# Optimization experiments

Measured on AMD Instinct MI355X. Metric: run time of the kernel, lower is better.

The kernel has to match this reference:

```python
import jax, jax.numpy as jnp
import numpy as np

NQ = 6          # num_qubits
BS = 3          # basis_size (Pauli x,y,z)
HID = 32        # LSTM hidden size
SNAPS = 16      # max_num_snapshots
BATCH = 1024
DIM = 2 ** NQ   # 64


def _pauli():
    sx = np.array([[0., 1.], [1., 0.]], dtype=np.complex64)
    sy = np.array([[0., -1j], [1j, 0.]], dtype=np.complex64)
    sz = np.array([[1., 0.], [0., -1.]], dtype=np.complex64)
    return np.stack([sx, sy, sz], axis=0)


def setup_inputs():
    key = jax.random.key(0)
    ks = jax.random.split(key, 12)
    snapshot = jax.random.uniform(ks[0], (BATCH, NQ), jnp.float32, -1.0, 1.0)
    basis_comp_vector = jax.nn.softmax(
        jax.random.normal(ks[1], (BATCH, NQ, BS), jnp.float32), axis=-1)
    # valid density matrices: rho = A A^dag / tr
    ar = jax.random.normal(ks[2], (BATCH, DIM, DIM), jnp.float32)
    ai = jax.random.normal(ks[3], (BATCH, DIM, DIM), jnp.float32)
    A = ar + 1j * ai
    rho_c = jnp.einsum('bij,bkj->bik', A, jnp.conj(A))
    tr = jnp.trace(rho_c, axis1=1, axis2=2)[:, None, None]
    rho_c = rho_c / tr
    rho = jnp.stack([jnp.real(rho_c), jnp.imag(rho_c)], axis=1).astype(jnp.float32)
    h0 = jax.random.normal(ks[4], (BATCH, HID), jnp.float32)
    c0 = jax.random.normal(ks[5], (BATCH, HID), jnp.float32)
    in_dim = NQ + NQ * BS
    W_ih = jax.random.normal(ks[6], (4 * HID, in_dim), jnp.float32) * 0.1
    W_hh = jax.random.normal(ks[7], (4 * HID, HID), jnp.float32) * 0.1
    b_ih = jax.random.normal(ks[8], (4 * HID,), jnp.float32) * 0.05
    b_hh = jax.random.normal(ks[9], (4 * HID,), jnp.float32) * 0.05
    Wp = jax.random.normal(ks[10], (NQ, HID, BS), jnp.float32) * 0.1
    bp = jax.random.normal(ks[11], (NQ, BS), jnp.float32) * 0.05
    pauli = _pauli()
    basis_r = jnp.asarray(np.real(pauli), jnp.float32)
    basis_i = jnp.asarray(np.imag(pauli), jnp.float32)
    return {"snapshot": snapshot, "basis_comp_vector": basis_comp_vector,
            "rho": rho, "h0": h0, "c0": c0,
            "W_ih": W_ih, "W_hh": W_hh, "b_ih": b_ih, "b_hh": b_hh,
            "Wp": Wp, "bp": bp, "basis_r": basis_r, "basis_i": basis_i}


def _apply(p, M, axis, b):
    # apply 2x2 batched operator M [b,2,2] on tensor axis `axis` of p [b]+(2,)*2NQ
    pm = jnp.moveaxis(p, axis, 1)
    shp = pm.shape
    out = jnp.einsum('bij,bjr->bir', M, pm.reshape(b, 2, -1)).reshape(shp)
    return jnp.moveaxis(out, 1, axis)


def _measure(rho_t, probs, basis, basis_c, b):
    # sequential single-qubit measurement on the collapsing mixed state
    pc = probs.astype(jnp.complex64)
    M = jnp.einsum('bqs,sij->bqij', pc, basis)    # prob-mixed basis ops
    Mc = jnp.einsum('bqs,sij->bqij', pc, basis_c)
    p = rho_t
    outs = []
    for q in range(NQ):
        p = _apply(p, M[:, q], 1 + q, b)          # row index of qubit q
        p = _apply(p, Mc[:, q], 1 + NQ + q, b)    # col index of qubit q
        tr = jnp.trace(p.reshape(b, DIM, DIM), axis1=1, axis2=2)
        outs.append(jnp.real(tr))                 # measurement value s
        p = p / tr.reshape((b,) + (1,) * (2 * NQ))  # renormalized post-state
    return jnp.stack(outs, axis=1)                 # [b, NQ]


def _forward(snapshot, basis_comp_vector, rho, h0, c0,
             W_ih, W_hh, b_ih, b_hh, Wp, bp, basis_r, basis_i):
    b = snapshot.shape[0]
    basis = (basis_r + 1j * basis_i).astype(jnp.complex64)
    basis_c = jnp.conj(basis)
    rho_t = (rho[:, 0] + 1j * rho[:, 1]).astype(jnp.complex64)
    rho_t = rho_t.reshape((b,) + (2,) * (2 * NQ))

    x = jnp.concatenate([snapshot, basis_comp_vector.reshape(b, -1)], axis=-1)
    feats = [x]
    h, c = h0, c0
    for _ in range(SNAPS - 1):
        # torch LSTMCell: gate order i, f, g, o
        g = x @ W_ih.T + b_ih + h @ W_hh.T + b_hh
        gi, gf, gg, go = jnp.split(g, 4, axis=-1)
        c = jax.nn.sigmoid(gf) * c + jax.nn.sigmoid(gi) * jnp.tanh(gg)
        h = jax.nn.sigmoid(go) * jnp.tanh(c)
        probs = jax.nn.softmax(jnp.einsum('bh,qhs->bqs', h, Wp) + bp, axis=-1)
        # torch.Tensor(snapshot_batch) detaches -> stop_gradient
        snaps = jax.lax.stop_gradient(_measure(rho_t, probs, basis, basis_c, b))
        x = jnp.concatenate([snaps, probs.reshape(b, -1)], axis=-1)
        feats.append(x)

    # classical-shadow reconstruction: kron_q (I + 3 s_q B_q)/2, averaged
    eye2 = jnp.eye(2, dtype=jnp.complex64)
    acc = jnp.zeros((b, DIM, DIM), jnp.complex64)
    last_bv = None
    for xw in feats:
        shadow = xw[:, :NQ]
        bv = xw[:, NQ:].reshape(b, NQ, BS)
        last_bv = bv
        Bq = jnp.einsum('bqs,sij->bqij', bv.astype(jnp.complex64), basis)
        rc = (eye2 + 3.0 * shadow[:, :, None, None].astype(jnp.complex64) * Bq) / 2.0
        k = rc[:, 0]
        dd = 2
        for q in range(1, NQ):  # batched kron chain
            k = jnp.einsum('bij,bkl->bikjl', k, rc[:, q]).reshape(b, dd * 2, dd * 2)
            dd *= 2
        acc = acc + k
    rho_rec = acc / SNAPS
    out = jnp.stack([jnp.real(rho_rec), jnp.imag(rho_rec)], axis=1)
    return out, last_bv


def reference(snapshot, basis_comp_vector, rho, h0, c0,
              W_ih, W_hh, b_ih, b_hh, Wp, bp, basis_r, basis_i):
    return _forward(snapshot, basis_comp_vector, rho, h0, c0,
                    W_ih, W_hh, b_ih, b_hh, Wp, bp, basis_r, basis_i)
```

## Files before the change

kernel.cpp:

```cpp
#include <hip/hip_runtime.h>

#define NQ 6
#define HID 32
#define SNAPS 16
#define BATCH 1024
#define FSTRIDE 24
#define FTOT 384
#define KSTR 24
#define KF   192

typedef float vfloat4 __attribute__((ext_vector_type(4)));

__device__ __forceinline__ float sigm_f(float x) { return 1.0f / (1.0f + __expf(-x)); }
__device__ __forceinline__ float tanh_f(float x) { return 1.0f - 2.0f / (__expf(2.0f * x) + 1.0f); }

__device__ __forceinline__ void rc_entry(float g, float b0, float b1, float b2,
                                         int i, int j, float& re, float& im) {
    if (i == j) { re = 0.5f + (i ? -g * b2 : g * b2); im = 0.0f; }
    else        { re = g * b0;  im = (i ? g * b1 : -g * b1); }
}

__global__ __launch_bounds__(256, 2)
void fused_kernel(const float* __restrict__ snapshot,
                  const float* __restrict__ bcv,
                  const float* __restrict__ h0,
                  const float* __restrict__ c0,
                  const float* __restrict__ W_ih,
                  const float* __restrict__ W_hh,
                  const float* __restrict__ b_ih,
                  const float* __restrict__ b_hh,
                  const float* __restrict__ Wp,
                  const float* __restrict__ bp,
                  float* __restrict__ out,
                  float* __restrict__ out_tail)
{
    __shared__ __align__(16) float sKA[16 * KF];
    __shared__ __align__(16) float sKB[16 * KF];
    __shared__ __align__(16) float feat[FTOT];
    __shared__ __align__(16) float sh[HID];
    __shared__ __align__(16) float sg[128];
    __shared__ __align__(16) float sWpT[18 * 36];
    __shared__ float sbp[18];

    const int b = blockIdx.x;
    const int t = threadIdx.x;

    float4 wih[6], whh[8];
    float bias = 0.0f, c = 0.0f;
    if (t < 128) {
        const float4* p = (const float4*)(W_ih + t * 24);
        #pragma unroll
        for (int k = 0; k < 6; ++k) wih[k] = p[k];
        const float4* q = (const float4*)(W_hh + t * 32);
        #pragma unroll
        for (int k = 0; k < 8; ++k) whh[k] = q[k];
        bias = b_ih[t] + b_hh[t];
    }
    for (int idx = t; idx < NQ * HID * 3; idx += 256) {
        int q = idx / 96, r = idx - q * 96;
        int h = r / 3, s = r - h * 3;
        sWpT[(q * 3 + s) * 36 + h] = Wp[idx];
    }
    if (t < 18) sbp[t] = bp[t];
    if (t < 32) { c = c0[b * 32 + t]; sh[t] = h0[b * 32 + t]; }
    if (t < 24) feat[t] = (t < 6) ? snapshot[b * 6 + t] : bcv[b * 18 + (t - 6)];
    __syncthreads();

    for (int step = 0; step < SNAPS - 1; ++step) {
        if (t < 128) {
            const float4* x4 = (const float4*)(feat + step * FSTRIDE);
            const float4* h4 = (const float4*)sh;
            float ga = bias, gb = 0.0f;
            #pragma unroll
            for (int k = 0; k < 6; ++k) {
                float4 xq = x4[k];
                ga += xq.x * wih[k].x + xq.y * wih[k].y;
                gb += xq.z * wih[k].z + xq.w * wih[k].w;
            }
            #pragma unroll
            for (int k = 0; k < 8; ++k) {
                float4 hq = h4[k];
                ga += hq.x * whh[k].x + hq.y * whh[k].y;
                gb += hq.z * whh[k].z + hq.w * whh[k].w;
            }
            sg[t] = ga + gb;
        }
        __syncthreads();

        if (t < 64) {
            if (t < 32) {
                float gi = sg[t], gf = sg[32 + t], gg = sg[64 + t], go = sg[96 + t];
                c = sigm_f(gf) * c + sigm_f(gi) * tanh_f(gg);
                sh[t] = sigm_f(go) * tanh_f(c);
            }
            __builtin_amdgcn_wave_barrier();
            int row = (t < 18) ? t : 17;
            const float4* wr  = (const float4*)&sWpT[row * 36];
            const float4* h4b = (const float4*)sh;
            float la = (t < 18) ? sbp[row] : 0.0f, lb = 0.0f;
            #pragma unroll
            for (int k = 0; k < 8; ++k) {
                float4 hq = h4b[k], wq = wr[k];
                la += hq.x * wq.x + hq.y * wq.y;
                lb += hq.z * wq.z + hq.w * wq.w;
            }
            float logit = la + lb;
            int q3 = 3 * (t < 6 ? t : 0);
            float l0 = __shfl(logit, q3), l1 = __shfl(logit, q3 + 1), l2 = __shfl(logit, q3 + 2);
            if (t < 6) {
                float m = fmaxf(l0, fmaxf(l1, l2));
                float e0 = __expf(l0 - m), e1 = __expf(l1 - m), e2 = __expf(l2 - m);
                float inv = 1.0f / (e0 + e1 + e2);
                float p0 = e0 * inv, p1 = e1 * inv, p2 = e2 * inv;
                float snap = p0 * p0 + p1 * p1 + p2 * p2;
                float* fd = feat + (step + 1) * FSTRIDE;
                fd[t] = snap;
                fd[6 + 3 * t]     = p0;
                fd[6 + 3 * t + 1] = p1;
                fd[6 + 3 * t + 2] = p2;
            }
        }
        __syncthreads();
    }

    if (t < 18) out_tail[b * 18 + t] = feat[15 * FSTRIDE + 6 + t];

    for (int n = t; n < 2048; n += 256) {
        int f = n >> 7, r = n & 127;
        int half = r >> 6, a = r & 63;
        const float* fx = &feat[f * FSTRIDE];
        int i0 = (a >> 5) & 1, i1 = (a >> 4) & 1, i2 = (a >> 3) & 1;
        int j0 = (a >> 2) & 1, j1 = (a >> 1) & 1, j2 = a & 1;
        int q = 3 * half;
        float g0 = 1.5f * fx[q], g1 = 1.5f * fx[q + 1], g2 = 1.5f * fx[q + 2];
        const float* bb = fx + 6 + 3 * q;
        float r0, m0, r1, m1, r2, m2;
        rc_entry(g0, bb[0], bb[1], bb[2], i0, j0, r0, m0);
        rc_entry(g1, bb[3], bb[4], bb[5], i1, j1, r1, m1);
        rc_entry(g2, bb[6], bb[7], bb[8], i2, j2, r2, m2);
        float pr = r0 * r1 - m0 * m1, pi = r0 * m1 + m0 * r1;
        float qr = pr * r2 - pi * m2, qi = pr * m2 + pi * r2;
        int row = a >> 3, col = a & 7;
        if (half == 0) {
            int off = f * KF + col * KSTR + ((row & 1) ? (7 + row) : row);
            sKA[off] = qr; sKA[off + 1] = qi;
        } else {
            int off = f * KF + row * KSTR + 2 * col;
            sKB[off] = qr; sKB[off + 1] = qi;
        }
    }
    __syncthreads();

    const int u = t & 15, v = t >> 4;
    const float* baseA = sKA + (u >> 1) * KSTR + 8 * (v >> 3);
    const float* baseB = sKB + (v & 7) * KSTR + 8 * (u & 1);
    float accr[4][4], acci[4][4];
    #pragma unroll
    for (int e = 0; e < 4; ++e)
        #pragma unroll
        for (int d = 0; d < 4; ++d) { accr[e][d] = 0.0f; acci[e][d] = 0.0f; }

    #pragma unroll 2
    for (int f = 0; f < SNAPS; ++f) {
        float4 A0 = *(const float4*)(baseA + f * KF);
        float4 A1 = *(const float4*)(baseA + f * KF + 4);
        float4 B0 = *(const float4*)(baseB + f * KF);
        float4 B1 = *(const float4*)(baseB + f * KF + 4);
        float ar[4] = {A0.x, A0.z, A1.x, A1.z};
        float ai[4] = {A0.y, A0.w, A1.y, A1.w};
        float br[4] = {B0.x, B0.z, B1.x, B1.z};
        float bi[4] = {B0.y, B0.w, B1.y, B1.w};
        #pragma unroll
        for (int e = 0; e < 4; ++e)
            #pragma unroll
            for (int d = 0; d < 4; ++d) {
                accr[e][d] += ar[e] * br[d] - ai[e] * bi[d];
                acci[e][d] += ar[e] * bi[d] + ai[e] * br[d];
            }
    }

    const float s = 1.0f / 16.0f;
    float* outb = out + (size_t)b * 8192;
    #pragma unroll
    for (int e = 0; e < 4; ++e) {
        int i = v + 16 * e;
        vfloat4 r4 = { accr[e][0] * s, accr[e][1] * s, accr[e][2] * s, accr[e][3] * s };
        vfloat4 i4 = { acci[e][0] * s, acci[e][1] * s, acci[e][2] * s, acci[e][3] * s };
        __builtin_nontemporal_store(r4, (vfloat4*)(outb + i * 64 + 4 * u));
        __builtin_nontemporal_store(i4, (vfloat4*)(outb + 4096 + i * 64 + 4 * u));
    }
}

extern "C" void kernel_launch(void* const* d_in, const int* in_sizes, int n_in,
                              void* d_out, int out_size, void* d_ws, size_t ws_size,
                              hipStream_t stream) {
    const float* snapshot = (const float*)d_in[0];
    const float* bcv      = (const float*)d_in[1];
    const float* h0       = (const float*)d_in[3];
    const float* c0       = (const float*)d_in[4];
    const float* W_ih     = (const float*)d_in[5];
    const float* W_hh     = (const float*)d_in[6];
    const float* b_ih     = (const float*)d_in[7];
    const float* b_hh     = (const float*)d_in[8];
    const float* Wp       = (const float*)d_in[9];
    const float* bp       = (const float*)d_in[10];
    float* out = (float*)d_out;

    fused_kernel<<<BATCH, 256, 0, stream>>>(
        snapshot, bcv, h0, c0, W_ih, W_hh, b_ih, b_hh, Wp, bp,
        out, out + (size_t)BATCH * 8192);
}
```

Baseline: 133.4 us.

## Process two batch elements per block and use packed float2 math

Result: no change. 135.8 us (+1.8%).

```diff
diff --git a/kernel.cpp b/kernel.cpp
--- a/kernel.cpp
+++ b/kernel.cpp
@@ -9,6 +9,7 @@
 #define KSTR 24
 #define KF   192
 
+typedef float v2f __attribute__((ext_vector_type(2)));
 typedef float vfloat4 __attribute__((ext_vector_type(4)));
 
 __device__ __forceinline__ float sigm_f(float x) { return 1.0f / (1.0f + __expf(-x)); }
@@ -36,158 +37,159 @@
 {
     __shared__ __align__(16) float sKA[16 * KF];
     __shared__ __align__(16) float sKB[16 * KF];
-    __shared__ __align__(16) float feat[FTOT];
-    __shared__ __align__(16) float sh[HID];
-    __shared__ __align__(16) float sg[128];
+    __shared__ __align__(16) float feat[2][FTOT];
+    __shared__ __align__(16) float sh[2][HID];
+    __shared__ __align__(16) float sg[2][128];
     __shared__ __align__(16) float sWpT[18 * 36];
     __shared__ float sbp[18];
 
-    const int b = blockIdx.x;
-    const int t = threadIdx.x;
-
-    float4 wih[6], whh[8];
-    float bias = 0.0f, c = 0.0f;
-    if (t < 128) {
-        const float4* p = (const float4*)(W_ih + t * 24);
-        #pragma unroll
-        for (int k = 0; k < 6; ++k) wih[k] = p[k];
-        const float4* q = (const float4*)(W_hh + t * 32);
-        #pragma unroll
-        for (int k = 0; k < 8; ++k) whh[k] = q[k];
-        bias = b_ih[t] + b_hh[t];
-    }
+    const int t    = threadIdx.x;
+    const int w    = t >> 6;
+    const int lane = t & 63;
+    const int e1   = w >> 1;
+    const int wl   = w & 1;
+    const int b0   = blockIdx.x * 2;
+    const int row  = wl * 64 + lane;
+
+    v2f wih[12], whh[16];
+    {
+        const v2f* p = (const v2f*)(W_ih + row * 24);
+        #pragma unroll
+        for (int k = 0; k < 12; ++k) wih[k] = p[k];
+        const v2f* q = (const v2f*)(W_hh + row * 32);
+        #pragma unroll
+        for (int k = 0; k < 16; ++k) whh[k] = q[k];
+    }
+    const float bias = b_ih[row] + b_hh[row];
+
     for (int idx = t; idx < NQ * HID * 3; idx += 256) {
         int q = idx / 96, r = idx - q * 96;
         int h = r / 3, s = r - h * 3;
         sWpT[(q * 3 + s) * 36 + h] = Wp[idx];
     }
     if (t < 18) sbp[t] = bp[t];
-    if (t < 32) { c = c0[b * 32 + t]; sh[t] = h0[b * 32 + t]; }
-    if (t < 24) feat[t] = (t < 6) ? snapshot[b * 6 + t] : bcv[b * 18 + (t - 6)];
+
+    float c = 0.0f;
+    if (wl == 0) {
+        if (lane < 32) { c = c0[(b0 + e1) * 32 + lane]; sh[e1][lane] = h0[(b0 + e1) * 32 + lane]; }
+        if (lane < 24)
+            feat[e1][lane] = (lane < 6) ? snapshot[(b0 + e1) * 6 + lane]
+                                        : bcv[(b0 + e1) * 18 + (lane - 6)];
+    }
     __syncthreads();
 
     for (int step = 0; step < SNAPS - 1; ++step) {
-        if (t < 128) {
-            const float4* x4 = (const float4*)(feat + step * FSTRIDE);
-            const float4* h4 = (const float4*)sh;
-            float ga = bias, gb = 0.0f;
-            #pragma unroll
-            for (int k = 0; k < 6; ++k) {
-                float4 xq = x4[k];
-                ga += xq.x * wih[k].x + xq.y * wih[k].y;
-                gb += xq.z * wih[k].z + xq.w * wih[k].w;
-            }
-            #pragma unroll
-            for (int k = 0; k < 8; ++k) {
-                float4 hq = h4[k];
-                ga += hq.x * whh[k].x + hq.y * whh[k].y;
-                gb += hq.z * whh[k].z + hq.w * whh[k].w;
-            }
-            sg[t] = ga + gb;
-        }
-        __syncthreads();
-
-        if (t < 64) {
-            if (t < 32) {
-                float gi = sg[t], gf = sg[32 + t], gg = sg[64 + t], go = sg[96 + t];
+        {
+            const v2f* x2 = (const v2f*)(feat[e1] + step * FSTRIDE);
+            const v2f* h2 = (const v2f*)sh[e1];
+            v2f g2 = {0.0f, 0.0f};
+            #pragma unroll
+            for (int k = 0; k < 12; ++k) g2 += x2[k] * wih[k];
+            #pragma unroll
+            for (int k = 0; k < 16; ++k) g2 += h2[k] * whh[k];
+            sg[e1][row] = bias + g2.x + g2.y;
+        }
+        __syncthreads();
+
+        if (wl == 0) {
+            if (lane < 32) {
+                float gi = sg[e1][lane],      gf = sg[e1][32 + lane];
+                float gg = sg[e1][64 + lane], go = sg[e1][96 + lane];
                 c = sigm_f(gf) * c + sigm_f(gi) * tanh_f(gg);
-                sh[t] = sigm_f(go) * tanh_f(c);
+                sh[e1][lane] = sigm_f(go) * tanh_f(c);
             }
             __builtin_amdgcn_wave_barrier();
-            int row = (t < 18) ? t : 17;
-            const float4* wr  = (const float4*)&sWpT[row * 36];
-            const float4* h4b = (const float4*)sh;
-            float la = (t < 18) ? sbp[row] : 0.0f, lb = 0.0f;
-            #pragma unroll
-            for (int k = 0; k < 8; ++k) {
-                float4 hq = h4b[k], wq = wr[k];
-                la += hq.x * wq.x + hq.y * wq.y;
-                lb += hq.z * wq.z + hq.w * wq.w;
+            int rr = (lane < 18) ? lane : 17;
+            const v2f* wr = (const v2f*)&sWpT[rr * 36];
+            const v2f* h2 = (const v2f*)sh[e1];
+            v2f l2 = {0.0f, 0.0f};
+            #pragma unroll
+            for (int k = 0; k < 16; ++k) l2 += h2[k] * wr[k];
+            float logit = ((lane < 18) ? sbp[rr] : 0.0f) + l2.x + l2.y;
+            int q3 = 3 * (lane < 6 ? lane : 0);
+            float l0 = __shfl(logit, q3), l1 = __shfl(logit, q3 + 1), l2s = __shfl(logit, q3 + 2);
+            if (lane < 6) {
+                float m = fmaxf(l0, fmaxf(l1, l2s));
+                float e0 = __expf(l0 - m), e1x = __expf(l1 - m), e2 = __expf(l2s - m);
+                float inv = 1.0f / (e0 + e1x + e2);
+                float p0 = e0 * inv, p1 = e1x * inv, p2 = e2 * inv;
+                float snap = p0 * p0 + p1 * p1 + p2 * p2;
+                float* fd = feat[e1] + (step + 1) * FSTRIDE;
+                fd[lane] = snap;
+                fd[6 + 3 * lane]     = p0;
+                fd[6 + 3 * lane + 1] = p1;
+                fd[6 + 3 * lane + 2] = p2;
             }
-            float logit = la + lb;
-            int q3 = 3 * (t < 6 ? t : 0);
-            float l0 = __shfl(logit, q3), l1 = __shfl(logit, q3 + 1), l2 = __shfl(logit, q3 + 2);
-            if (t < 6) {
-                float m = fmaxf(l0, fmaxf(l1, l2));
-                float e0 = __expf(l0 - m), e1 = __expf(l1 - m), e2 = __expf(l2 - m);
-                float inv = 1.0f / (e0 + e1 + e2);
-                float p0 = e0 * inv, p1 = e1 * inv, p2 = e2 * inv;
-                float snap = p0 * p0 + p1 * p1 + p2 * p2;
-                float* fd = feat + (step + 1) * FSTRIDE;
-                fd[t] = snap;
-                fd[6 + 3 * t]     = p0;
-                fd[6 + 3 * t + 1] = p1;
-                fd[6 + 3 * t + 2] = p2;
-            }
-        }
-        __syncthreads();
-    }
-
-    if (t < 18) out_tail[b * 18 + t] = feat[15 * FSTRIDE + 6 + t];
-
-    for (int n = t; n < 2048; n += 256) {
-        int f = n >> 7, r = n & 127;
-        int half = r >> 6, a = r & 63;
-        const float* fx = &feat[f * FSTRIDE];
-        int i0 = (a >> 5) & 1, i1 = (a >> 4) & 1, i2 = (a >> 3) & 1;
-        int j0 = (a >> 2) & 1, j1 = (a >> 1) & 1, j2 = a & 1;
-        int q = 3 * half;
-        float g0 = 1.5f * fx[q], g1 = 1.5f * fx[q + 1], g2 = 1.5f * fx[q + 2];
-        const float* bb = fx + 6 + 3 * q;
-        float r0, m0, r1, m1, r2, m2;
-        rc_entry(g0, bb[0], bb[1], bb[2], i0, j0, r0, m0);
-        rc_entry(g1, bb[3], bb[4], bb[5], i1, j1, r1, m1);
-        rc_entry(g2, bb[6], bb[7], bb[8], i2, j2, r2, m2);
-        float pr = r0 * r1 - m0 * m1, pi = r0 * m1 + m0 * r1;
-        float qr = pr * r2 - pi * m2, qi = pr * m2 + pi * r2;
-        int row = a >> 3, col = a & 7;
-        if (half == 0) {
-            int off = f * KF + col * KSTR + ((row & 1) ? (7 + row) : row);
-            sKA[off] = qr; sKA[off + 1] = qi;
-        } else {
-            int off = f * KF + row * KSTR + 2 * col;
-            sKB[off] = qr; sKB[off + 1] = qi;
-        }
-    }
-    __syncthreads();
+        }
+        __syncthreads();
+    }
+
+    if (wl == 0 && lane < 18)
+        out_tail[(b0 + e1) * 18 + lane] = feat[e1][15 * FSTRIDE + 6 + lane];
 
     const int u = t & 15, v = t >> 4;
     const float* baseA = sKA + (u >> 1) * KSTR + 8 * (v >> 3);
     const float* baseB = sKB + (v & 7) * KSTR + 8 * (u & 1);
-    float accr[4][4], acci[4][4];
-    #pragma unroll
-    for (int e = 0; e < 4; ++e)
-        #pragma unroll
-        for (int d = 0; d < 4; ++d) { accr[e][d] = 0.0f; acci[e][d] = 0.0f; }
-
-    #pragma unroll 2
-    for (int f = 0; f < SNAPS; ++f) {
-        float4 A0 = *(const float4*)(baseA + f * KF);
-        float4 A1 = *(const float4*)(baseA + f * KF + 4);
-        float4 B0 = *(const float4*)(baseB + f * KF);
-        float4 B1 = *(const float4*)(baseB + f * KF + 4);
-        float ar[4] = {A0.x, A0.z, A1.x, A1.z};
-        float ai[4] = {A0.y, A0.w, A1.y, A1.w};
-        float br[4] = {B0.x, B0.z, B1.x, B1.z};
-        float bi[4] = {B0.y, B0.w, B1.y, B1.w};
-        #pragma unroll
-        for (int e = 0; e < 4; ++e)
-            #pragma unroll
-            for (int d = 0; d < 4; ++d) {
-                accr[e][d] += ar[e] * br[d] - ai[e] * bi[d];
-                acci[e][d] += ar[e] * bi[d] + ai[e] * br[d];
+
+    for (int e = 0; e < 2; ++e) {
+        __syncthreads();
+
+        for (int n = t; n < 2048; n += 256) {
+            int f = n >> 7, r = n & 127;
+            int half = r >> 6, a = r & 63;
+            const float* fx = &feat[e][f * FSTRIDE];
+            int i0 = (a >> 5) & 1, i1 = (a >> 4) & 1, i2 = (a >> 3) & 1;
+            int j0 = (a >> 2) & 1, j1 = (a >> 1) & 1, j2 = a & 1;
+            int q = 3 * half;
+            float g0 = 1.5f * fx[q], g1 = 1.5f * fx[q + 1], g2 = 1.5f * fx[q + 2];
+            const float* bb = fx + 6 + 3 * q;
+            float r0, m0, r1, m1, r2, m2;
+            rc_entry(g0, bb[0], bb[1], bb[2], i0, j0, r0, m0);
+            rc_entry(g1, bb[3], bb[4], bb[5], i1, j1, r1, m1);
+            rc_entry(g2, bb[6], bb[7], bb[8], i2, j2, r2, m2);
+            float pr = r0 * r1 - m0 * m1, pi = r0 * m1 + m0 * r1;
+            float qr = pr * r2 - pi * m2, qi = pr * m2 + pi * r2;
+            int rw = a >> 3, col = a & 7;
+            if (half == 0) {
+                int off = f * KF + col * KSTR + ((rw & 1) ? (7 + rw) : rw);
+                sKA[off] = qr; sKA[off + 1] = qi;
+            } else {
+                int off = f * KF + rw * KSTR + 2 * col;
+                sKB[off] = qr; sKB[off + 1] = qi;
             }
-    }
-
-    const float s = 1.0f / 16.0f;
-    float* outb = out + (size_t)b * 8192;
-    #pragma unroll
-    for (int e = 0; e < 4; ++e) {
-        int i = v + 16 * e;
-        vfloat4 r4 = { accr[e][0] * s, accr[e][1] * s, accr[e][2] * s, accr[e][3] * s };
-        vfloat4 i4 = { acci[e][0] * s, acci[e][1] * s, acci[e][2] * s, acci[e][3] * s };
-        __builtin_nontemporal_store(r4, (vfloat4*)(outb + i * 64 + 4 * u));
-        __builtin_nontemporal_store(i4, (vfloat4*)(outb + 4096 + i * 64 + 4 * u));
+        }
+        __syncthreads();
+
+        v2f acc[4][4];
+        #pragma unroll
+        for (int k = 0; k < 4; ++k)
+            #pragma unroll
+            for (int d = 0; d < 4; ++d) acc[k][d] = (v2f){0.0f, 0.0f};
+
+        #pragma unroll 2
+        for (int f = 0; f < SNAPS; ++f) {
+            const v2f* A = (const v2f*)(baseA + f * KF);
+            const v2f* B = (const v2f*)(baseB + f * KF);
+            v2f a0 = A[0], a1 = A[1], a2 = A[2], a3 = A[3];
+            v2f bq0 = B[0], bq1 = B[1], bq2 = B[2], bq3 = B[3];
+            #define CMAC(k, a, d, b)                                   \
+                acc[k][d] += (a).x * (b) + ((v2f){-(a).y, (a).y}) * (b).yx;
+            #define CROW(k, a)  CMAC(k,a,0,bq0) CMAC(k,a,1,bq1) CMAC(k,a,2,bq2) CMAC(k,a,3,bq3)
+            CROW(0, a0) CROW(1, a1) CROW(2, a2) CROW(3, a3)
+            #undef CROW
+            #undef CMAC
+        }
+
+        const float s = 1.0f / 16.0f;
+        float* outb = out + (size_t)(b0 + e) * 8192;
+        #pragma unroll
+        for (int k = 0; k < 4; ++k) {
+            int i = v + 16 * k;
+            vfloat4 r4 = { acc[k][0].x * s, acc[k][1].x * s, acc[k][2].x * s, acc[k][3].x * s };
+            vfloat4 i4 = { acc[k][0].y * s, acc[k][1].y * s, acc[k][2].y * s, acc[k][3].y * s };
+            __builtin_nontemporal_store(r4, (vfloat4*)(outb + i * 64 + 4 * u));
+            __builtin_nontemporal_store(i4, (vfloat4*)(outb + 4096 + i * 64 + 4 * u));
+        }
     }
 }
 
@@ -206,7 +208,7 @@
     const float* bp       = (const float*)d_in[10];
     float* out = (float*)d_out;
 
-    fused_kernel<<<BATCH, 256, 0, stream>>>(
+    fused_kernel<<<BATCH / 2, 256, 0, stream>>>(
         snapshot, bcv, h0, c0, W_ih, W_hh, b_ih, b_hh, Wp, bp,
         out, out + (size_t)BATCH * 8192);
 }
```

## Run LSTM recurrence in a single wavefront and pack complex MACs

Applied to the files above, without the earlier changes.

New measurement: 149.2 us. 1.12x slower.

```diff
diff --git a/kernel.cpp b/kernel.cpp
--- a/kernel.cpp
+++ b/kernel.cpp
@@ -9,6 +9,7 @@
 #define KSTR 24
 #define KF   192
 
+typedef float v2f __attribute__((ext_vector_type(2)));
 typedef float vfloat4 __attribute__((ext_vector_type(4)));
 
 __device__ __forceinline__ float sigm_f(float x) { return 1.0f / (1.0f + __expf(-x)); }
@@ -20,7 +21,7 @@
     else        { re = g * b0;  im = (i ? g * b1 : -g * b1); }
 }
 
-__global__ __launch_bounds__(256, 2)
+__global__ __launch_bounds__(256, 1)
 void fused_kernel(const float* __restrict__ snapshot,
                   const float* __restrict__ bcv,
                   const float* __restrict__ h0,
@@ -38,66 +39,73 @@
     __shared__ __align__(16) float sKB[16 * KF];
     __shared__ __align__(16) float feat[FTOT];
     __shared__ __align__(16) float sh[HID];
-    __shared__ __align__(16) float sg[128];
     __shared__ __align__(16) float sWpT[18 * 36];
     __shared__ float sbp[18];
 
     const int b = blockIdx.x;
     const int t = threadIdx.x;
 
-    float4 wih[6], whh[8];
-    float bias = 0.0f, c = 0.0f;
-    if (t < 128) {
-        const float4* p = (const float4*)(W_ih + t * 24);
-        #pragma unroll
-        for (int k = 0; k < 6; ++k) wih[k] = p[k];
-        const float4* q = (const float4*)(W_hh + t * 32);
-        #pragma unroll
-        for (int k = 0; k < 8; ++k) whh[k] = q[k];
-        bias = b_ih[t] + b_hh[t];
-    }
     for (int idx = t; idx < NQ * HID * 3; idx += 256) {
         int q = idx / 96, r = idx - q * 96;
         int h = r / 3, s = r - h * 3;
         sWpT[(q * 3 + s) * 36 + h] = Wp[idx];
     }
-    if (t < 18) sbp[t] = bp[t];
-    if (t < 32) { c = c0[b * 32 + t]; sh[t] = h0[b * 32 + t]; }
-    if (t < 24) feat[t] = (t < 6) ? snapshot[b * 6 + t] : bcv[b * 18 + (t - 6)];
+    if (t >= 64 && t < 82) sbp[t - 64] = bp[t - 64];
+
+    float4 wih0[6], wih1[6], whh0[8], whh1[8];
+    float bias0 = 0.0f, bias1 = 0.0f, c = 0.0f;
+    if (t < 64) {
+        const float4* p0 = (const float4*)(W_ih + t * 24);
+        const float4* p1 = (const float4*)(W_ih + (t + 64) * 24);
+        #pragma unroll
+        for (int k = 0; k < 6; ++k) { wih0[k] = p0[k]; wih1[k] = p1[k]; }
+        const float4* q0 = (const float4*)(W_hh + t * 32);
+        const float4* q1 = (const float4*)(W_hh + (t + 64) * 32);
+        #pragma unroll
+        for (int k = 0; k < 8; ++k) { whh0[k] = q0[k]; whh1[k] = q1[k]; }
+        bias0 = b_ih[t] + b_hh[t];
+        bias1 = b_ih[t + 64] + b_hh[t + 64];
+        if (t < 32) { c = c0[b * 32 + t]; sh[t] = h0[b * 32 + t]; }
+        if (t < 24) feat[t] = (t < 6) ? snapshot[b * 6 + t] : bcv[b * 18 + (t - 6)];
+    }
     __syncthreads();
 
-    for (int step = 0; step < SNAPS - 1; ++step) {
-        if (t < 128) {
+    if (t < 64) {
+        const int l = t;
+        for (int step = 0; step < SNAPS - 1; ++step) {
             const float4* x4 = (const float4*)(feat + step * FSTRIDE);
             const float4* h4 = (const float4*)sh;
-            float ga = bias, gb = 0.0f;
+            float g0 = bias0, g1 = bias1, g0b = 0.0f, g1b = 0.0f;
             #pragma unroll
             for (int k = 0; k < 6; ++k) {
                 float4 xq = x4[k];
-                ga += xq.x * wih[k].x + xq.y * wih[k].y;
-                gb += xq.z * wih[k].z + xq.w * wih[k].w;
+                g0  += xq.x * wih0[k].x + xq.y * wih0[k].y;
+                g0b += xq.z * wih0[k].z + xq.w * wih0[k].w;
+                g1  += xq.x * wih1[k].x + xq.y * wih1[k].y;
+                g1b += xq.z * wih1[k].z + xq.w * wih1[k].w;
             }
             #pragma unroll
             for (int k = 0; k < 8; ++k) {
                 float4 hq = h4[k];
-                ga += hq.x * whh[k].x + hq.y * whh[k].y;
-                gb += hq.z * whh[k].z + hq.w * whh[k].w;
-            }
-            sg[t] = ga + gb;
-        }
-        __syncthreads();
-
-        if (t < 64) {
-            if (t < 32) {
-                float gi = sg[t], gf = sg[32 + t], gg = sg[64 + t], go = sg[96 + t];
-                c = sigm_f(gf) * c + sigm_f(gi) * tanh_f(gg);
-                sh[t] = sigm_f(go) * tanh_f(c);
+                g0  += hq.x * whh0[k].x + hq.y * whh0[k].y;
+                g0b += hq.z * whh0[k].z + hq.w * whh0[k].w;
+                g1  += hq.x * whh1[k].x + hq.y * whh1[k].y;
+                g1b += hq.z * whh1[k].z + hq.w * whh1[k].w;
+            }
+            g0 += g0b; g1 += g1b;
+
+            float gf = __shfl_xor(g0, 32);
+            float go = __shfl_xor(g1, 32);
+            if (l < 32) {
+                c = sigm_f(gf) * c + sigm_f(g0) * tanh_f(g1);
+                sh[l] = sigm_f(go) * tanh_f(c);
             }
             __builtin_amdgcn_wave_barrier();
-            int row = (t < 18) ? t : 17;
-            const float4* wr  = (const float4*)&sWpT[row * 36];
+
+            int rr = (l < 18) ? l : 17;
+            const float4* wr  = (const float4*)&sWpT[rr * 36];
             const float4* h4b = (const float4*)sh;
-            float la = (t < 18) ? sbp[row] : 0.0f, lb = 0.0f;
+            float la = (l < 18) ? sbp[rr] : 0.0f, lb = 0.0f;
             #pragma unroll
             for (int k = 0; k < 8; ++k) {
                 float4 hq = h4b[k], wq = wr[k];
@@ -105,23 +113,24 @@
                 lb += hq.z * wq.z + hq.w * wq.w;
             }
             float logit = la + lb;
-            int q3 = 3 * (t < 6 ? t : 0);
+            int q3 = 3 * (l < 6 ? l : 0);
             float l0 = __shfl(logit, q3), l1 = __shfl(logit, q3 + 1), l2 = __shfl(logit, q3 + 2);
-            if (t < 6) {
+            if (l < 6) {
                 float m = fmaxf(l0, fmaxf(l1, l2));
                 float e0 = __expf(l0 - m), e1 = __expf(l1 - m), e2 = __expf(l2 - m);
                 float inv = 1.0f / (e0 + e1 + e2);
                 float p0 = e0 * inv, p1 = e1 * inv, p2 = e2 * inv;
                 float snap = p0 * p0 + p1 * p1 + p2 * p2;
                 float* fd = feat + (step + 1) * FSTRIDE;
-                fd[t] = snap;
-                fd[6 + 3 * t]     = p0;
-                fd[6 + 3 * t + 1] = p1;
-                fd[6 + 3 * t + 2] = p2;
-            }
+                fd[l] = snap;
+                fd[6 + 3 * l]     = p0;
+                fd[6 + 3 * l + 1] = p1;
+                fd[6 + 3 * l + 2] = p2;
+            }
+            __builtin_amdgcn_wave_barrier();
         }
-        __syncthreads();
-    }
+    }
+    __syncthreads();
 
     if (t < 18) out_tail[b * 18 + t] = feat[15 * FSTRIDE + 6 + t];
 
@@ -154,38 +163,34 @@
     const int u = t & 15, v = t >> 4;
     const float* baseA = sKA + (u >> 1) * KSTR + 8 * (v >> 3);
     const float* baseB = sKB + (v & 7) * KSTR + 8 * (u & 1);
-    float accr[4][4], acci[4][4];
+
+    v2f acc[4][4];
     #pragma unroll
-    for (int e = 0; e < 4; ++e)
+    for (int k = 0; k < 4; ++k)
         #pragma unroll
-        for (int d = 0; d < 4; ++d) { accr[e][d] = 0.0f; acci[e][d] = 0.0f; }
+        for (int d = 0; d < 4; ++d) acc[k][d] = (v2f){0.0f, 0.0f};
 
     #pragma unroll 2
     for (int f = 0; f < SNAPS; ++f) {
-        float4 A0 = *(const float4*)(baseA + f * KF);
-        float4 A1 = *(const float4*)(baseA + f * KF + 4);
-        float4 B0 = *(const float4*)(baseB + f * KF);
-        float4 B1 = *(const float4*)(baseB + f * KF + 4);
-        float ar[4] = {A0.x, A0.z, A1.x, A1.z};
-        float ai[4] = {A0.y, A0.w, A1.y, A1.w};
-        float br[4] = {B0.x, B0.z, B1.x, B1.z};
-        float bi[4] = {B0.y, B0.w, B1.y, B1.w};
-        #pragma unroll
-        for (int e = 0; e < 4; ++e)
-            #pragma unroll
-            for (int d = 0; d < 4; ++d) {
-                accr[e][d] += ar[e] * br[d] - ai[e] * bi[d];
-                acci[e][d] += ar[e] * bi[d] + ai[e] * br[d];
-            }
+        const v2f* A = (const v2f*)(baseA + f * KF);
+        const v2f* B = (const v2f*)(baseB + f * KF);
+        v2f a0 = A[0], a1 = A[1], a2 = A[2], a3 = A[3];
+        v2f bq0 = B[0], bq1 = B[1], bq2 = B[2], bq3 = B[3];
+        #define CMAC(k, a, d, b)                                   \
+            acc[k][d] += (a).x * (b) + ((v2f){-(a).y, (a).y}) * (b).yx;
+        #define CROW(k, a)  CMAC(k,a,0,bq0) CMAC(k,a,1,bq1) CMAC(k,a,2,bq2) CMAC(k,a,3,bq3)
+        CROW(0, a0) CROW(1, a1) CROW(2, a2) CROW(3, a3)
+        #undef CROW
+        #undef CMAC
     }
 
     const float s = 1.0f / 16.0f;
     float* outb = out + (size_t)b * 8192;
     #pragma unroll
-    for (int e = 0; e < 4; ++e) {
-        int i = v + 16 * e;
-        vfloat4 r4 = { accr[e][0] * s, accr[e][1] * s, accr[e][2] * s, accr[e][3] * s };
-        vfloat4 i4 = { acci[e][0] * s, acci[e][1] * s, acci[e][2] * s, acci[e][3] * s };
+    for (int k = 0; k < 4; ++k) {
+        int i = v + 16 * k;
+        vfloat4 r4 = { acc[k][0].x * s, acc[k][1].x * s, acc[k][2].x * s, acc[k][3].x * s };
+        vfloat4 i4 = { acc[k][0].y * s, acc[k][1].y * s, acc[k][2].y * s, acc[k][3].y * s };
         __builtin_nontemporal_store(r4, (vfloat4*)(outb + i * 64 + 4 * u));
         __builtin_nontemporal_store(i4, (vfloat4*)(outb + 4096 + i * 64 + 4 * u));
     }
```
